# Kernel optimization log

Hardware: AMD Instinct MI355X
Metric: run time of the kernel (lower is better)

Reference implementation:

```python
import jax, jax.numpy as jnp
import numpy as np
from jax import lax

BN_EPS = 1e-5

def _bn(x, g, b):
    # eval-mode BatchNorm with default running stats (mean=0, var=1)
    sh = (1, -1) + (1,) * (x.ndim - 2)
    return x * (g / jnp.sqrt(1.0 + BN_EPS)).reshape(sh) + b.reshape(sh)

def _simam(x, lam=1e-4):
    axes = tuple(range(2, x.ndim))
    mu = x.mean(axis=axes, keepdims=True)
    d2 = (x - mu) ** 2
    var = d2.mean(axis=axes, keepdims=True)
    e = d2 / (2.0 * var + 1e-12) + lam
    return jax.nn.sigmoid(1.0 / (e + 1e-12)) * x

def _dwconv1d(x, w, pad, groups):
    return lax.conv_general_dilated(
        x, w, (1,), [(pad, pad)],
        dimension_numbers=('NCH', 'OIH', 'NCH'),
        feature_group_count=groups)

def _adaptive_pool_matrix(t_in, t_out):
    # torch AdaptiveAvgPool1d: window i = [floor(i*t_in/t_out), ceil((i+1)*t_in/t_out))
    M = np.zeros((t_in, t_out), dtype=np.float32)
    for i in range(t_out):
        s = (i * t_in) // t_out
        e = -(-((i + 1) * t_in) // t_out)
        M[s:e, i] = 1.0 / (e - s)
    return jnp.asarray(M)

def _deform_conv1d(x, w, ow, ob):
    # depthwise deformable conv1d, padding='valid'; grid_sample bilinear,
    # zeros padding, align_corners=True -> pure 1D bilinear gather at pos.
    B, C, T = x.shape
    K = w.shape[1]
    T_out = T - K + 1
    off = _dwconv1d(x, ow, 0, C) + ob[None, :, None]        # (B, C*K, T_out)
    off = off.reshape(B, C, K, T_out)
    pos = (jnp.arange(T_out, dtype=x.dtype)[None, None, None, :]
           + jnp.arange(K, dtype=x.dtype)[None, None, :, None] + off)
    i0f = jnp.floor(pos)
    f = pos - i0f
    i0 = i0f.astype(jnp.int32)
    xb = jnp.broadcast_to(x[:, :, None, :], (B, C, K, T))
    def gather(idx):
        valid = (idx >= 0) & (idx < T)
        v = jnp.take_along_axis(xb, jnp.clip(idx, 0, T - 1), axis=3)
        return jnp.where(valid, v, 0.0)
    samp = gather(i0) * (1.0 - f) + gather(i0 + 1) * f      # (B,C,K,T_out)
    return jnp.einsum('bckt,ck->bct', samp, w)

def _branch(x, sw, g1, b1, tw, g2, b2):
    # spatial depthwise conv (kernel covers full channel axis) -> (B,5,T)
    h = jnp.einsum('bcht,ch->bct', x, sw)
    h = _simam(jax.nn.elu(_bn(h, g1, b1)))
    h = _dwconv1d(h, tw, tw.shape[-1] // 2, h.shape[1])     # temporal depthwise, same length
    return _simam(jax.nn.elu(_bn(h, g2, b2)))

def setup_inputs() -> dict:
    key = jax.random.key(0)
    ks = iter(jax.random.split(key, 48))
    B, C_in, T, n_class = 256, 22, 1000, 4
    k1, k2, k3 = 15, 31, 63  # _odd(round(fs*{0.06,0.12,0.25})), fs=250
    def rn(shape, scale=0.1):
        return scale * jax.random.normal(next(ks), shape, dtype=jnp.float32)
    inp = {'x': jax.random.normal(next(ks), (B, 1, C_in, T), dtype=jnp.float32),
           'stem_w': rn((15, 1, 2, 3)),
           'stem_g': 1.0 + rn((15,)), 'stem_b': rn((15,))}
    for i, kt in zip((1, 2, 3), (k1, k2, k3)):
        inp[f'b{i}_sw'] = rn((5, C_in))
        inp[f'b{i}_g1'] = 1.0 + rn((5,)); inp[f'b{i}_b1'] = rn((5,))
        inp[f'b{i}_tw'] = rn((5, 1, kt))
        inp[f'b{i}_g2'] = 1.0 + rn((5,)); inp[f'b{i}_b2'] = rn((5,))
    inp['pw_w'] = rn((5, 15))
    inp['pw_g'] = 1.0 + rn((5,)); inp['pw_b'] = rn((5,))
    inp['d1_w'] = rn((5, 5));  inp['d1_ow'] = rn((25, 1, 5), 0.02);  inp['d1_ob'] = jnp.zeros((25,), jnp.float32)
    inp['d2_w'] = rn((5, 10)); inp['d2_ow'] = rn((50, 1, 10), 0.02); inp['d2_ob'] = jnp.zeros((50,), jnp.float32)
    inp['fc_w'] = rn((n_class, 5 * 25)); inp['fc_b'] = rn((n_class,))
    return inp

def reference(x, stem_w, stem_g, stem_b,
              b1_sw, b1_g1, b1_b1, b1_tw, b1_g2, b1_b2,
              b2_sw, b2_g1, b2_b1, b2_tw, b2_g2, b2_b2,
              b3_sw, b3_g1, b3_b1, b3_tw, b3_g2, b3_b2,
              pw_w, pw_g, pw_b,
              d1_w, d1_ow, d1_ob, d2_w, d2_ow, d2_ob,
              fc_w, fc_b):
    # stem: conv2d k=(2,3) 'same' (torch pads extra on the right for even k)
    h = lax.conv_general_dilated(x, stem_w, (1, 1), [(0, 1), (1, 1)],
                                 dimension_numbers=('NCHW', 'OIHW', 'NCHW'))
    h = jax.nn.elu(_bn(h, stem_g, stem_b))                  # (B,15,22,T); dropout = eval no-op
    o1 = _branch(h[:, 0:5],  b1_sw, b1_g1, b1_b1, b1_tw, b1_g2, b1_b2)
    o2 = _branch(h[:, 5:10], b2_sw, b2_g1, b2_b1, b2_tw, b2_g2, b2_b2)
    o3 = _branch(h[:, 10:15], b3_sw, b3_g1, b3_b1, b3_tw, b3_g2, b3_b2)
    hc = jnp.concatenate([o1, o2, o3], axis=1)              # (B,15,T)
    hc = jnp.einsum('bct,to->bco', hc, _adaptive_pool_matrix(hc.shape[-1], 40))
    hc = jnp.einsum('bct,oc->bot', hc, pw_w)                # 1x1 pointwise
    hc = _simam(jax.nn.elu(_bn(hc, pw_g, pw_b)))            # (B,5,40)
    hc = _deform_conv1d(hc, d1_w, d1_ow, d1_ob)             # (B,5,36)
    hc = _deform_conv1d(hc, d2_w, d2_ow, d2_ob)             # (B,5,27)
    hc = jnp.einsum('bct,to->bco', hc, _adaptive_pool_matrix(hc.shape[-1], 25))
    return hc.reshape(hc.shape[0], -1) @ fc_w.T + fc_b      # (B,n_class)
```

## Files before the change

### kernel.cpp

```cpp
#include <hip/hip_runtime.h>
#include <math.h>

#define BNS 0.99999500003749972f

__device__ __forceinline__ float eluf(float v) {
    return v > 0.f ? v : (__expf(v) - 1.f);
}
__device__ __forceinline__ float sigmf(float u) {
    return 1.f / (1.f + __expf(-u));
}
__device__ __forceinline__ float sgpr(float v) {
    return __int_as_float(__builtin_amdgcn_readfirstlane(__float_as_int(v)));
}

#define PSTR 1024
#define PADZ 32
#define ZLEN 1120

__device__ __forceinline__ void block_reduce2(float& s1, float& s2, float* red) {
#pragma unroll
    for (int m = 32; m > 0; m >>= 1) {
        s1 += __shfl_xor(s1, m, 64);
        s2 += __shfl_xor(s2, m, 64);
    }
    const int wid = threadIdx.x >> 6, lane = threadIdx.x & 63;
    if (lane == 0) { red[wid * 2] = s1; red[wid * 2 + 1] = s2; }
    __syncthreads();
    s1 = red[0] + red[2] + red[4] + red[6];
    s2 = red[1] + red[3] + red[5] + red[7];
}

__global__ __launch_bounds__(256) void k_stem(
    const float* __restrict__ x,
    const float* __restrict__ stem_w,
    const float* __restrict__ stem_g, const float* __restrict__ stem_b,
    const float* __restrict__ sw1, const float* __restrict__ sw2, const float* __restrict__ sw3,
    float* __restrict__ pre)
{
    const int tid = threadIdx.x;
    const int g = blockIdx.y;
    const int b = blockIdx.z;
    const int t = blockIdx.x * 256 + tid;
    float* prow0 = pre + (b * 15 + g * 5) * PSTR + t;

    if (t >= 1000) {
#pragma unroll
        for (int c = 0; c < 5; ++c) prow0[c * PSTR] = 0.f;
        return;
    }

    const float* xb = x + b * 22000;
    const bool lo = (t == 0), hi = (t == 999);
    const float mlo = lo ? 0.f : 1.f, mhi = hi ? 0.f : 1.f;
    const float* pm = xb + (lo ? t : t - 1);
    const float* pc = xb + t;
    const float* pp = xb + (hi ? t : t + 1);

    const float* swp = (g == 0 ? sw1 : g == 1 ? sw2 : sw3);
    float w[5][6], gs[5], bs[5];
#pragma unroll
    for (int c = 0; c < 5; ++c) {
        const int C = g * 5 + c;
#pragma unroll
        for (int j = 0; j < 6; ++j) w[c][j] = sgpr(stem_w[C * 6 + j]);
        gs[c] = sgpr(stem_g[C] * BNS);
        bs[c] = sgpr(stem_b[C]);
    }

    float acc[5] = {0.f, 0.f, 0.f, 0.f, 0.f};
    float c0 = pm[0] * mlo, c1 = pc[0], c2 = pp[0] * mhi;
    float n0, n1, n2;
#pragma unroll
    for (int i = 0; i < 22; ++i) {
        if (i < 21) {
            const int ro = (i + 1) * 1000;
            n0 = pm[ro] * mlo; n1 = pc[ro]; n2 = pp[ro] * mhi;
        } else {
            n0 = n1 = n2 = 0.f;
        }
#pragma unroll
        for (int c = 0; c < 5; ++c) {
            float v = w[c][0] * c0 + w[c][1] * c1 + w[c][2] * c2
                    + w[c][3] * n0 + w[c][4] * n1 + w[c][5] * n2;
            v = eluf(v * gs[c] + bs[c]);
            acc[c] += v * sgpr(swp[c * 22 + i]);
        }
        c0 = n0; c1 = n1; c2 = n2;
    }
#pragma unroll
    for (int c = 0; c < 5; ++c) prow0[c * PSTR] = acc[c];
}

template<int K>
__device__ __forceinline__ void branch_block(
    const float* __restrict__ row,
    float g1s, float b1v,
    float wreg,
    float g2s, float b2v,
    float* __restrict__ zrow,
    float* __restrict__ red,
    float* __restrict__ out40)
{
    const int tid = threadIdx.x;
    const int t0 = tid * 4;
    const bool act = tid < 250;

    if (tid < PADZ) zrow[tid] = 0.f;
    if (tid >= 32 && tid < 120) zrow[PADZ + 1000 + (tid - 32)] = 0.f;

    float y0 = 0.f, y1 = 0.f, y2 = 0.f, y3 = 0.f, s1 = 0.f, s2 = 0.f;
    if (act) {
        const float4 v = *reinterpret_cast<const float4*>(row + t0);
        y0 = eluf(v.x * g1s + b1v);
        y1 = eluf(v.y * g1s + b1v);
        y2 = eluf(v.z * g1s + b1v);
        y3 = eluf(v.w * g1s + b1v);
        s1 = y0 + y1 + y2 + y3;
        s2 = y0 * y0 + y1 * y1 + y2 * y2 + y3 * y3;
    }
    block_reduce2(s1, s2, red);
    {
        const float mu = s1 * 1e-3f;
        const float var = s2 * 1e-3f - mu * mu;
        const float iv = 1.f / (2.f * var + 1e-12f);
        if (act) {
            float d;
            float4 z;
            d = y0 - mu; z.x = sigmf(1.f / (d * d * iv + 1e-4f + 1e-12f)) * y0;
            d = y1 - mu; z.y = sigmf(1.f / (d * d * iv + 1e-4f + 1e-12f)) * y1;
            d = y2 - mu; z.z = sigmf(1.f / (d * d * iv + 1e-4f + 1e-12f)) * y2;
            d = y3 - mu; z.w = sigmf(1.f / (d * d * iv + 1e-4f + 1e-12f)) * y3;
            *reinterpret_cast<float4*>(&zrow[PADZ + t0]) = z;
        }
    }
    __syncthreads();

    float a0 = 0.f, a1 = 0.f, a2 = 0.f, a3 = 0.f;
    if (act) {
        const int A = PADZ + t0 - (K / 2) - 1;
        float W[20];
#pragma unroll
        for (int q = 0; q < 5; ++q)
            *reinterpret_cast<float4*>(&W[q * 4]) = *reinterpret_cast<const float4*>(&zrow[A + q * 4]);

#pragma unroll
        for (int cb = 0; cb < K; cb += 16) {
            float P[16];
            if (cb + 16 < K) {
#pragma unroll
                for (int q = 0; q < 4; ++q)
                    *reinterpret_cast<float4*>(&P[q * 4]) =
                        *reinterpret_cast<const float4*>(&zrow[A + cb + 20 + q * 4]);
            }
            const int DD = (K - cb < 16) ? (K - cb) : 16;
#pragma unroll
            for (int dd = 0; dd < DD; ++dd) {
                const float wv = __shfl(wreg, cb + dd, 64);
                a0 += W[dd + 1] * wv;
                a1 += W[dd + 2] * wv;
                a2 += W[dd + 3] * wv;
                a3 += W[dd + 4] * wv;
            }
            if (cb + 16 < K) {
#pragma unroll
                for (int q = 0; q < 4; ++q) W[q] = W[16 + q];
#pragma unroll
                for (int q = 0; q < 16; ++q) W[4 + q] = P[q];
            }
        }
    }

    float u0 = 0.f, u1 = 0.f, u2 = 0.f, u3 = 0.f;
    s1 = 0.f; s2 = 0.f;
    if (act) {
        u0 = eluf(a0 * g2s + b2v);
        u1 = eluf(a1 * g2s + b2v);
        u2 = eluf(a2 * g2s + b2v);
        u3 = eluf(a3 * g2s + b2v);
        s1 = u0 + u1 + u2 + u3;
        s2 = u0 * u0 + u1 * u1 + u2 * u2 + u3 * u3;
    }
    block_reduce2(s1, s2, red);
    {
        const float mu = s1 * 1e-3f;
        const float var = s2 * 1e-3f - mu * mu;
        const float iv = 1.f / (2.f * var + 1e-12f);
        if (act) {
            float d;
            float4 z;
            d = u0 - mu; z.x = sigmf(1.f / (d * d * iv + 1e-4f + 1e-12f)) * u0;
            d = u1 - mu; z.y = sigmf(1.f / (d * d * iv + 1e-4f + 1e-12f)) * u1;
            d = u2 - mu; z.z = sigmf(1.f / (d * d * iv + 1e-4f + 1e-12f)) * u2;
            d = u3 - mu; z.w = sigmf(1.f / (d * d * iv + 1e-4f + 1e-12f)) * u3;
            *reinterpret_cast<float4*>(&zrow[PADZ + t0]) = z;
        }
    }
    __syncthreads();

    if (tid < 40) {
        float s = 0.f;
#pragma unroll
        for (int q = 0; q < 25; ++q) s += zrow[PADZ + tid * 25 + q];
        out40[tid] = s * (1.f / 25.f);
    }
}

__global__ __launch_bounds__(256) void k_branch(
    const float* __restrict__ pre,
    const float* __restrict__ g1a, const float* __restrict__ b1a,
    const float* __restrict__ tw1,
    const float* __restrict__ g2a, const float* __restrict__ b2a,
    const float* __restrict__ g1b, const float* __restrict__ b1b,
    const float* __restrict__ tw2,
    const float* __restrict__ g2b, const float* __restrict__ b2b,
    const float* __restrict__ g1c, const float* __restrict__ b1c,
    const float* __restrict__ tw3,
    const float* __restrict__ g2c, const float* __restrict__ b2c,
    float* __restrict__ pooled)
{
    __shared__ float zrow[ZLEN];
    __shared__ float red[8];

    const int row_id = blockIdx.x;
    const int C = row_id % 15;
    const int br = C / 5, c = C % 5;
    const int lane = threadIdx.x & 63;

    const float* row = pre + (size_t)row_id * PSTR;
    float* out40 = pooled + row_id * 40;

    if (br == 0) {
        const float wreg = (lane < 15) ? tw1[c * 15 + lane] : 0.f;
        branch_block<15>(row, g1a[c] * BNS, b1a[c], wreg, g2a[c] * BNS, b2a[c], zrow, red, out40);
    } else if (br == 1) {
        const float wreg = (lane < 31) ? tw2[c * 31 + lane] : 0.f;
        branch_block<31>(row, g1b[c] * BNS, b1b[c], wreg, g2b[c] * BNS, b2b[c], zrow, red, out40);
    } else {
        const float wreg = (lane < 63) ? tw3[c * 63 + lane] : 0.f;
        branch_block<63>(row, g1c[c] * BNS, b1c[c], wreg, g2c[c] * BNS, b2c[c], zrow, red, out40);
    }
}

__global__ __launch_bounds__(128) void k_head(
    const float* __restrict__ pooled,
    const float* __restrict__ pw_w, const float* __restrict__ pw_g, const float* __restrict__ pw_b,
    const float* __restrict__ d1_w, const float* __restrict__ d1_ow, const float* __restrict__ d1_ob,
    const float* __restrict__ d2_w, const float* __restrict__ d2_ow, const float* __restrict__ d2_ob,
    const float* __restrict__ fc_w, const float* __restrict__ fc_b,
    float* __restrict__ out)
{
    __shared__ float P[600];
    __shared__ float A[200];
    __shared__ float Bv[200];
    __shared__ float C1[180];
    __shared__ float C2[135];
    __shared__ float D[125];
    __shared__ float mu5[5], iv5[5];

    const int b = blockIdx.x, tid = threadIdx.x;

    for (int i = tid; i < 600; i += 128) P[i] = pooled[b * 600 + i];
    __syncthreads();

    for (int i = tid; i < 200; i += 128) {
        int o = i / 40, t = i % 40;
        float s = 0.f;
        for (int cc = 0; cc < 15; ++cc) s += P[cc * 40 + t] * pw_w[o * 15 + cc];
        float v = s * (pw_g[o] * BNS) + pw_b[o];
        A[i] = eluf(v);
    }
    __syncthreads();

    if (tid < 5) {
        float s = 0.f;
        for (int t = 0; t < 40; ++t) s += A[tid * 40 + t];
        float mu = s * (1.f / 40.f);
        float v2 = 0.f;
        for (int t = 0; t < 40; ++t) { float d = A[tid * 40 + t] - mu; v2 += d * d; }
        mu5[tid] = mu;
        iv5[tid] = 1.f / (2.f * (v2 * (1.f / 40.f)) + 1e-12f);
    }
    __syncthreads();

    for (int i = tid; i < 200; i += 128) {
        int o = i / 40;
        float a = A[i];
        float d = a - mu5[o];
        float e = d * d * iv5[o] + 1e-4f;
        Bv[i] = sigmf(1.f / (e + 1e-12f)) * a;
    }
    __syncthreads();

    for (int i = tid; i < 180; i += 128) {
        int cc = i / 36, t = i % 36;
        float o = 0.f;
        for (int k = 0; k < 5; ++k) {
            float off = d1_ob[cc * 5 + k];
            for (int d = 0; d < 5; ++d) off += Bv[cc * 40 + t + d] * d1_ow[(cc * 5 + k) * 5 + d];
            float pos = (float)(t + k) + off;
            float fl = floorf(pos);
            float f = pos - fl;
            int i0 = (int)fl;
            float v0 = (i0 >= 0 && i0 < 40) ? Bv[cc * 40 + i0] : 0.f;
            float v1 = (i0 + 1 >= 0 && i0 + 1 < 40) ? Bv[cc * 40 + i0 + 1] : 0.f;
            o += (v0 * (1.f - f) + v1 * f) * d1_w[cc * 5 + k];
        }
        C1[i] = o;
    }
    __syncthreads();

    for (int i = tid; i < 135; i += 128) {
        int cc = i / 27, t = i % 27;
        float o = 0.f;
        for (int k = 0; k < 10; ++k) {
            float off = d2_ob[cc * 10 + k];
            for (int d = 0; d < 10; ++d) off += C1[cc * 36 + t + d] * d2_ow[(cc * 10 + k) * 10 + d];
            float pos = (float)(t + k) + off;
            float fl = floorf(pos);
            float f = pos - fl;
            int i0 = (int)fl;
            float v0 = (i0 >= 0 && i0 < 36) ? C1[cc * 36 + i0] : 0.f;
            float v1 = (i0 + 1 >= 0 && i0 + 1 < 36) ? C1[cc * 36 + i0 + 1] : 0.f;
            o += (v0 * (1.f - f) + v1 * f) * d2_w[cc * 10 + k];
        }
        C2[i] = o;
    }
    __syncthreads();

    for (int i = tid; i < 125; i += 128) {
        int cc = i / 25, j = i % 25;
        int s0 = (j * 27) / 25;
        int e0 = ((j + 1) * 27 + 24) / 25;
        float s = 0.f;
        for (int q = s0; q < e0; ++q) s += C2[cc * 27 + q];
        D[i] = s / (float)(e0 - s0);
    }
    __syncthreads();

    if (tid < 64) {
        float part0 = 0.f, part1 = 0.f, part2 = 0.f, part3 = 0.f;
        for (int i = tid; i < 125; i += 64) {
            const float dv = D[i];
            part0 += dv * fc_w[0 * 125 + i];
            part1 += dv * fc_w[1 * 125 + i];
            part2 += dv * fc_w[2 * 125 + i];
            part3 += dv * fc_w[3 * 125 + i];
        }
#pragma unroll
        for (int m = 32; m > 0; m >>= 1) {
            part0 += __shfl_xor(part0, m, 64);
            part1 += __shfl_xor(part1, m, 64);
            part2 += __shfl_xor(part2, m, 64);
            part3 += __shfl_xor(part3, m, 64);
        }
        if (tid == 0) {
            out[b * 4 + 0] = part0 + fc_b[0];
            out[b * 4 + 1] = part1 + fc_b[1];
            out[b * 4 + 2] = part2 + fc_b[2];
            out[b * 4 + 3] = part3 + fc_b[3];
        }
    }
}

extern "C" void kernel_launch(void* const* d_in, const int* in_sizes, int n_in,
                              void* d_out, int out_size, void* d_ws, size_t ws_size,
                              hipStream_t stream) {
    const float* x      = (const float*)d_in[0];
    const float* stem_w = (const float*)d_in[1];
    const float* stem_g = (const float*)d_in[2];
    const float* stem_b = (const float*)d_in[3];
    const float* b1_sw = (const float*)d_in[4];
    const float* b1_g1 = (const float*)d_in[5];
    const float* b1_b1 = (const float*)d_in[6];
    const float* b1_tw = (const float*)d_in[7];
    const float* b1_g2 = (const float*)d_in[8];
    const float* b1_b2 = (const float*)d_in[9];
    const float* b2_sw = (const float*)d_in[10];
    const float* b2_g1 = (const float*)d_in[11];
    const float* b2_b1 = (const float*)d_in[12];
    const float* b2_tw = (const float*)d_in[13];
    const float* b2_g2 = (const float*)d_in[14];
    const float* b2_b2 = (const float*)d_in[15];
    const float* b3_sw = (const float*)d_in[16];
    const float* b3_g1 = (const float*)d_in[17];
    const float* b3_b1 = (const float*)d_in[18];
    const float* b3_tw = (const float*)d_in[19];
    const float* b3_g2 = (const float*)d_in[20];
    const float* b3_b2 = (const float*)d_in[21];
    const float* pw_w  = (const float*)d_in[22];
    const float* pw_g  = (const float*)d_in[23];
    const float* pw_b  = (const float*)d_in[24];
    const float* d1_w  = (const float*)d_in[25];
    const float* d1_ow = (const float*)d_in[26];
    const float* d1_ob = (const float*)d_in[27];
    const float* d2_w  = (const float*)d_in[28];
    const float* d2_ow = (const float*)d_in[29];
    const float* d2_ob = (const float*)d_in[30];
    const float* fc_w  = (const float*)d_in[31];
    const float* fc_b  = (const float*)d_in[32];

    float* pre    = (float*)d_ws;
    float* pooled = (float*)((char*)d_ws + (size_t)256 * 15 * PSTR * 4);

    k_stem<<<dim3(4, 3, 256), 256, 0, stream>>>(
        x, stem_w, stem_g, stem_b, b1_sw, b2_sw, b3_sw, pre);

    k_branch<<<3840, 256, 0, stream>>>(
        pre,
        b1_g1, b1_b1, b1_tw, b1_g2, b1_b2,
        b2_g1, b2_b1, b2_tw, b2_g2, b2_b2,
        b3_g1, b3_b1, b3_tw, b3_g2, b3_b2,
        pooled);

    k_head<<<256, 128, 0, stream>>>(
        pooled, pw_w, pw_g, pw_b,
        d1_w, d1_ow, d1_ob, d2_w, d2_ow, d2_ob,
        fc_w, fc_b, (float*)d_out);
}
```

Measured before the change: 81.80 us.

## Compute all 15 stem channels per block with an LDS-staged input tile

The stem kernel now processes all three channel groups in one block instead of launching one block per group. Each block stages a padded 22x258 input tile in shared memory, so the input is read from global memory once rather than three times. The BN scale is folded into the conv weights, and the spatial weights are broadcast through lane shuffles. The trade-off is higher register pressure from 15 accumulators and 90 weights, a non-unrolled row loop, and the padding columns of the output buffer no longer being zeroed.

Measured after the change: 86.55 us. 1.06x slower.

```diff
diff --git a/kernel.cpp b/kernel.cpp
--- a/kernel.cpp
+++ b/kernel.cpp
@@ -16,6 +16,7 @@
 #define PSTR 1024
 #define PADZ 32
 #define ZLEN 1120
+#define XSW 258
 
 __device__ __forceinline__ void block_reduce2(float& s1, float& s2, float* red) {
 #pragma unroll
@@ -37,58 +38,68 @@
     const float* __restrict__ sw1, const float* __restrict__ sw2, const float* __restrict__ sw3,
     float* __restrict__ pre)
 {
+    __shared__ float xs[22 * XSW];
     const int tid = threadIdx.x;
-    const int g = blockIdx.y;
-    const int b = blockIdx.z;
-    const int t = blockIdx.x * 256 + tid;
-    float* prow0 = pre + (b * 15 + g * 5) * PSTR + t;
-
-    if (t >= 1000) {
-#pragma unroll
-        for (int c = 0; c < 5; ++c) prow0[c * PSTR] = 0.f;
-        return;
-    }
-
+    const int lane = tid & 63;
+    const int tile0 = blockIdx.x * 256;
+    const int b = blockIdx.y;
     const float* xb = x + b * 22000;
-    const bool lo = (t == 0), hi = (t == 999);
-    const float mlo = lo ? 0.f : 1.f, mhi = hi ? 0.f : 1.f;
-    const float* pm = xb + (lo ? t : t - 1);
-    const float* pc = xb + t;
-    const float* pp = xb + (hi ? t : t + 1);
-
-    const float* swp = (g == 0 ? sw1 : g == 1 ? sw2 : sw3);
-    float w[5][6], gs[5], bs[5];
-#pragma unroll
-    for (int c = 0; c < 5; ++c) {
-        const int C = g * 5 + c;
-#pragma unroll
-        for (int j = 0; j < 6; ++j) w[c][j] = sgpr(stem_w[C * 6 + j]);
-        gs[c] = sgpr(stem_g[C] * BNS);
-        bs[c] = sgpr(stem_b[C]);
-    }
-
-    float acc[5] = {0.f, 0.f, 0.f, 0.f, 0.f};
-    float c0 = pm[0] * mlo, c1 = pc[0], c2 = pp[0] * mhi;
+
+    for (int idx = tid; idx < 22 * XSW; idx += 256) {
+        const int r = idx / XSW, k = idx - r * XSW;
+        const int gc = tile0 - 1 + k;
+        xs[idx] = (gc >= 0 && gc < 1000) ? xb[r * 1000 + gc] : 0.f;
+    }
+
+    float wrow[15];
+#pragma unroll
+    for (int cc = 0; cc < 15; ++cc) {
+        const float* swp = (cc < 5 ? sw1 : cc < 10 ? sw2 : sw3);
+        wrow[cc] = (lane < 22) ? swp[(cc % 5) * 22 + lane] : 0.f;
+    }
+
+    float w[15][6], bs[15];
+#pragma unroll
+    for (int cc = 0; cc < 15; ++cc) {
+        const float gsc = sgpr(stem_g[cc]) * BNS;
+#pragma unroll
+        for (int j = 0; j < 6; ++j) w[cc][j] = sgpr(stem_w[cc * 6 + j]) * gsc;
+        bs[cc] = sgpr(stem_b[cc]);
+    }
+
+    __syncthreads();
+
+    const int t = tile0 + tid;
+    if (t >= 1000) return;
+
+    float acc[15];
+#pragma unroll
+    for (int cc = 0; cc < 15; ++cc) acc[cc] = 0.f;
+
+    float c0 = xs[tid], c1 = xs[tid + 1], c2 = xs[tid + 2];
     float n0, n1, n2;
-#pragma unroll
+#pragma unroll 1
     for (int i = 0; i < 22; ++i) {
         if (i < 21) {
-            const int ro = (i + 1) * 1000;
-            n0 = pm[ro] * mlo; n1 = pc[ro]; n2 = pp[ro] * mhi;
+            const int rb = (i + 1) * XSW + tid;
+            n0 = xs[rb]; n1 = xs[rb + 1]; n2 = xs[rb + 2];
         } else {
             n0 = n1 = n2 = 0.f;
         }
 #pragma unroll
-        for (int c = 0; c < 5; ++c) {
-            float v = w[c][0] * c0 + w[c][1] * c1 + w[c][2] * c2
-                    + w[c][3] * n0 + w[c][4] * n1 + w[c][5] * n2;
-            v = eluf(v * gs[c] + bs[c]);
-            acc[c] += v * sgpr(swp[c * 22 + i]);
+        for (int cc = 0; cc < 15; ++cc) {
+            const float sv = __shfl(wrow[cc], i, 64);
+            float v = fmaf(w[cc][0], c0, fmaf(w[cc][1], c1, fmaf(w[cc][2], c2,
+                      fmaf(w[cc][3], n0, fmaf(w[cc][4], n1, fmaf(w[cc][5], n2, bs[cc]))))));
+            acc[cc] += eluf(v) * sv;
         }
         c0 = n0; c1 = n1; c2 = n2;
     }
-#pragma unroll
-    for (int c = 0; c < 5; ++c) prow0[c * PSTR] = acc[c];
+
+    float* prow = pre + (size_t)(b * 15) * PSTR + t;
+#pragma unroll
+    for (int cc = 0; cc < 15; ++cc)
+        prow[cc * PSTR] = acc[cc];
 }
 
 template<int K>
@@ -402,7 +413,7 @@
     float* pre    = (float*)d_ws;
     float* pooled = (float*)((char*)d_ws + (size_t)256 * 15 * PSTR * 4);
 
-    k_stem<<<dim3(4, 3, 256), 256, 0, stream>>>(
+    k_stem<<<dim3(4, 256), 256, 0, stream>>>(
         x, stem_w, stem_g, stem_b, b1_sw, b2_sw, b3_sw, pre);
 
     k_branch<<<3840, 256, 0, stream>>>(
```
